# Kernel optimization log

Measured on AMD Instinct MI355X. Metric: run time of the kernel, lower is better.

Reference implementation:

```python
import jax, jax.numpy as jnp
import numpy as np

N = 100000
E = 1600000
IN_DIM, FEAT, HID, OUT = 128, 64, 64, 64


def setup_inputs() -> dict:
    key = jax.random.key(0)
    ks = jax.random.split(key, 12)
    x = jax.random.normal(ks[0], (N, IN_DIM), dtype=jnp.float32)
    edge_index = jax.random.randint(ks[1], (2, E), 0, N, dtype=jnp.int64)
    def lin(k, fan_in, fan_out):
        s = 1.0 / np.sqrt(fan_in)
        kw, kb = jax.random.split(k)
        W = jax.random.uniform(kw, (fan_in, fan_out), jnp.float32, -s, s)
        b = jax.random.uniform(kb, (fan_out,), jnp.float32, -s, s)
        return W, b
    W_pre, b_pre = lin(ks[2], IN_DIM, FEAT)
    W1, b1 = lin(ks[3], FEAT, HID)
    Wh, bh = lin(ks[4], HID, HID)
    Wo, bo = lin(ks[5], HID, OUT)
    return {"x": x, "edge_index": edge_index,
            "W_pre": W_pre, "b_pre": b_pre,
            "W1": W1, "b1": b1, "Wh": Wh, "bh": bh,
            "Wo": Wo, "bo": bo}


def _gcn_conv(x, W, b, src, dst, norm, n):
    # linear transform then normalized scatter-add aggregation at dst
    h = x @ W                           # [N, out]
    msg = h[src] * norm[:, None]        # [E+N, out] gather + scale
    out = jax.ops.segment_sum(msg, dst, num_segments=n)
    return out + b


def reference(x, edge_index, W_pre, b_pre, W1, b1, Wh, bh, Wo, bo):
    n = x.shape[0]
    loop = jnp.arange(n, dtype=edge_index.dtype)
    src = jnp.concatenate([edge_index[0], loop])  # self-loops appended
    dst = jnp.concatenate([edge_index[1], loop])
    deg = jax.ops.segment_sum(jnp.ones_like(dst, x.dtype), dst, num_segments=n)
    dinv = jnp.where(deg > 0, jax.lax.rsqrt(deg), 0.0)
    norm = dinv[src] * dinv[dst]        # symmetric D^-1/2 A_hat D^-1/2

    h = x @ W_pre + b_pre               # feature_pre linear
    h = jax.nn.relu(_gcn_conv(h, W1, b1, src, dst, norm, n))
    # dropout is identity in eval mode
    h = jax.nn.relu(_gcn_conv(h, Wh, bh, src, dst, norm, n))
    h = _gcn_conv(h, Wo, bo, src, dst, norm, n)
    # row-wise L2 normalize (F.normalize, eps=1e-12)
    nrm = jnp.maximum(jnp.linalg.norm(h, axis=-1, keepdims=True), 1e-12)
    return h / nrm
```

## Files before the change

kernel.cpp:

```cpp
#include <hip/hip_runtime.h>
#include <hip/hip_fp16.h>

#define N_DIM 128
#define F_DIM 64
#define NB 256
#define TILE 2048
#define BCAP 8192

typedef _Float16 half8 __attribute__((ext_vector_type(8)));
typedef float f32x4 __attribute__((ext_vector_type(4)));

__global__ __launch_bounds__(256) void k_compose(const float* __restrict__ Wpre, const float* __restrict__ W1,
                                                 const float* __restrict__ bpre, float* __restrict__ Wc,
                                                 float* __restrict__ bb) {
    int c = threadIdx.x & 63;
    int rq = threadIdx.x >> 6;
    for (int r = rq; r < N_DIM; r += 4) {
        float acc = 0.f;
        for (int k = 0; k < 64; ++k) acc = fmaf(Wpre[r * 64 + k], W1[k * 64 + c], acc);
        Wc[r * 64 + c] = acc;
    }
    if (rq == 0) {
        float acc = 0.f;
        for (int k = 0; k < 64; ++k) acc = fmaf(bpre[k], W1[k * 64 + c], acc);
        bb[c] = acc;
    }
}

__global__ __launch_bounds__(256) void k_bucket(const int* __restrict__ src, const int* __restrict__ dst,
                                                int* __restrict__ bsrc, int* __restrict__ bdst,
                                                int* __restrict__ bcnt, int e, unsigned int magic, int cap) {
    __shared__ int hist[NB], lofs[NB], gbase[NB], lcur[NB];
    __shared__ int as_[TILE], ad_[TILE];
    __shared__ unsigned char ab_[TILE];
    int tid = threadIdx.x;
    for (int t0 = blockIdx.x * TILE; t0 < e; t0 += gridDim.x * TILE) {
        int cnt = min(TILE, e - t0);
        hist[tid] = 0;
        __syncthreads();
        int dv[8], sv[8], bv[8];
#pragma unroll
        for (int j = 0; j < 8; ++j) {
            int local = j * 256 + tid;
            int idx = t0 + local;
            bool ok = local < cnt;
            dv[j] = ok ? __builtin_nontemporal_load(dst + idx) : 0;
            sv[j] = ok ? __builtin_nontemporal_load(src + idx) : 0;
            bv[j] = ok ? (int)(((unsigned long long)(unsigned)dv[j] * magic) >> 32) : -1;
            if (ok) atomicAdd(&hist[bv[j]], 1);
        }
        __syncthreads();
        int v = hist[tid];
        lofs[tid] = v;
        __syncthreads();
        for (int o = 1; o < NB; o <<= 1) {
            int x = (tid >= o) ? lofs[tid - o] : 0;
            __syncthreads();
            lofs[tid] += x;
            __syncthreads();
        }
        int excl = lofs[tid] - v;
        lofs[tid] = excl;
        lcur[tid] = excl;
        gbase[tid] = atomicAdd(&bcnt[tid], v);
        __syncthreads();
#pragma unroll
        for (int j = 0; j < 8; ++j) {
            if (bv[j] >= 0) {
                int pos = atomicAdd(&lcur[bv[j]], 1);
                as_[pos] = sv[j];
                ad_[pos] = dv[j];
                ab_[pos] = (unsigned char)bv[j];
            }
        }
        __syncthreads();
        for (int k = tid; k < cnt; k += 256) {
            int p = ab_[k];
            size_t gi = (size_t)p * cap + gbase[p] + (k - lofs[p]);
            bsrc[gi] = as_[k];
            bdst[gi] = ad_[k];
        }
        __syncthreads();
    }
}

__global__ __launch_bounds__(256) void k_sort(const int* __restrict__ bsrc, const int* __restrict__ bdst,
                                              const int* __restrict__ bcnt,
                                              float* __restrict__ dinv, int* __restrict__ start,
                                              int* __restrict__ srcs, int cap, int nchunk, int n, int e) {
    __shared__ int sb[NB];
    __shared__ int lcnt[512], lcur[512];
    __shared__ int out[BCAP];
    int t = threadIdx.x;
    int b = blockIdx.x;
    int bc = bcnt[t];
    sb[t] = bc;
    __syncthreads();
    for (int o = 1; o < NB; o <<= 1) {
        int x = (t >= o) ? sb[t - o] : 0;
        __syncthreads();
        sb[t] += x;
        __syncthreads();
    }
    int base = sb[b] - bcnt[b];
    if (b == 0 && t == 0) start[n] = e;
    __syncthreads();

    int len = min(bcnt[b], min(cap, BCAP));
    int d0 = b * nchunk;
    int nloc = min(nchunk, n - d0);
    lcnt[t] = 0; lcnt[t + 256] = 0;
    __syncthreads();
    const int* bd = bdst + (size_t)b * cap;
    const int* bs = bsrc + (size_t)b * cap;
    for (int i = t; i < len; i += 256) atomicAdd(&lcnt[bd[i] - d0], 1);
    __syncthreads();
    int sv0 = lcnt[t], sv1 = lcnt[t + 256];
    for (int o = 1; o < 512; o <<= 1) {
        int x0 = (t >= o) ? lcnt[t - o] : 0;
        int x1 = (t + 256 >= o) ? lcnt[t + 256 - o] : 0;
        __syncthreads();
        lcnt[t] += x0;
        lcnt[t + 256] += x1;
        __syncthreads();
    }
    int ex0 = lcnt[t] - sv0;
    int ex1 = lcnt[t + 256] - sv1;
    lcur[t] = ex0; lcur[t + 256] = ex1;
    if (t < nloc) { start[d0 + t] = base + ex0; dinv[d0 + t] = rsqrtf((float)sv0 + 1.0f); }
    if (t + 256 < nloc) { start[d0 + t + 256] = base + ex1; dinv[d0 + t + 256] = rsqrtf((float)sv1 + 1.0f); }
    __syncthreads();
    for (int i = t; i < len; i += 256) {
        int d = bd[i] - d0;
        int pos = atomicAdd(&lcur[d], 1);
        out[pos] = bs[i];
    }
    __syncthreads();
    for (int k = t; k < len; k += 256) srcs[base + k] = out[k];
}


template <int S>
__device__ inline void pack_w(const float* __restrict__ W, half8* __restrict__ Bf) {
    for (int f = threadIdx.x; f < S * 4 * 64; f += 256) {
        int l = f & 63, c = (f >> 6) & 3, s = f >> 8;
        int kbase = s * 32 + ((l >> 4) << 3);
        int col = c * 16 + (l & 15);
        half8 pk;
#pragma unroll
        for (int i = 0; i < 8; ++i) pk[i] = (_Float16)W[(kbase + i) * 64 + col];
        Bf[f] = pk;
    }
    __syncthreads();
}

__global__ __launch_bounds__(256) void k_gemm_f(const float* __restrict__ X, const float* __restrict__ Wc,
                                                const float* __restrict__ bb, const float* __restrict__ dinv,
                                                __half* __restrict__ U, int n) {
    __shared__ half8 Bf[4 * 4 * 64];
    pack_w<4>(Wc, Bf);
    int lane = threadIdx.x & 63;
    int row = lane & 15, kq = lane >> 4;
    float bbv0 = bb[0 * 16 + row], bbv1 = bb[1 * 16 + row], bbv2 = bb[2 * 16 + row], bbv3 = bb[3 * 16 + row];
    int gw = (blockIdx.x * 256 + threadIdx.x) >> 6;
    int nw = (gridDim.x * 256) >> 6;
    int ntile = n >> 4;
    for (int tile = gw; tile < ntile; tile += nw) {
        int r0 = tile << 4;
        const float* xp = X + (size_t)(r0 + row) * N_DIM + (kq << 3);
        f32x4 ac0 = {0.f, 0.f, 0.f, 0.f}, ac1 = ac0, ac2 = ac0, ac3 = ac0;
#pragma unroll
        for (int s = 0; s < 4; ++s) {
            float4 lo = *(const float4*)(xp + s * 32);
            float4 hi = *(const float4*)(xp + s * 32 + 4);
            half8 a;
            a[0] = (_Float16)lo.x; a[1] = (_Float16)lo.y; a[2] = (_Float16)lo.z; a[3] = (_Float16)lo.w;
            a[4] = (_Float16)hi.x; a[5] = (_Float16)hi.y; a[6] = (_Float16)hi.z; a[7] = (_Float16)hi.w;
            ac0 = __builtin_amdgcn_mfma_f32_16x16x32_f16(a, Bf[(s * 4 + 0) * 64 + lane], ac0, 0, 0, 0);
            ac1 = __builtin_amdgcn_mfma_f32_16x16x32_f16(a, Bf[(s * 4 + 1) * 64 + lane], ac1, 0, 0, 0);
            ac2 = __builtin_amdgcn_mfma_f32_16x16x32_f16(a, Bf[(s * 4 + 2) * 64 + lane], ac2, 0, 0, 0);
            ac3 = __builtin_amdgcn_mfma_f32_16x16x32_f16(a, Bf[(s * 4 + 3) * 64 + lane], ac3, 0, 0, 0);
        }
        int rbase = r0 + (kq << 2);
        float d0 = dinv[rbase + 0], d1 = dinv[rbase + 1], d2 = dinv[rbase + 2], d3 = dinv[rbase + 3];
        __half* up = U + (size_t)rbase * F_DIM + row;
        up[0 * F_DIM +  0] = __float2half(d0 * (ac0[0] + bbv0));
        up[1 * F_DIM +  0] = __float2half(d1 * (ac0[1] + bbv0));
        up[2 * F_DIM +  0] = __float2half(d2 * (ac0[2] + bbv0));
        up[3 * F_DIM +  0] = __float2half(d3 * (ac0[3] + bbv0));
        up[0 * F_DIM + 16] = __float2half(d0 * (ac1[0] + bbv1));
        up[1 * F_DIM + 16] = __float2half(d1 * (ac1[1] + bbv1));
        up[2 * F_DIM + 16] = __float2half(d2 * (ac1[2] + bbv1));
        up[3 * F_DIM + 16] = __float2half(d3 * (ac1[3] + bbv1));
        up[0 * F_DIM + 32] = __float2half(d0 * (ac2[0] + bbv2));
        up[1 * F_DIM + 32] = __float2half(d1 * (ac2[1] + bbv2));
        up[2 * F_DIM + 32] = __float2half(d2 * (ac2[2] + bbv2));
        up[3 * F_DIM + 32] = __float2half(d3 * (ac2[3] + bbv2));
        up[0 * F_DIM + 48] = __float2half(d0 * (ac3[0] + bbv3));
        up[1 * F_DIM + 48] = __float2half(d1 * (ac3[1] + bbv3));
        up[2 * F_DIM + 48] = __float2half(d2 * (ac3[2] + bbv3));
        up[3 * F_DIM + 48] = __float2half(d3 * (ac3[3] + bbv3));
    }
}

__global__ __launch_bounds__(256) void k_gemm_l(const __half* __restrict__ H, const float* __restrict__ W,
                                                const float* __restrict__ dinv, __half* __restrict__ U, int n) {
    __shared__ half8 Bf[2 * 4 * 64];
    pack_w<2>(W, Bf);
    int lane = threadIdx.x & 63;
    int row = lane & 15, kq = lane >> 4;
    int gw = (blockIdx.x * 256 + threadIdx.x) >> 6;
    int nw = (gridDim.x * 256) >> 6;
    int ntile = n >> 4;
    for (int tile = gw; tile < ntile; tile += nw) {
        int r0 = tile << 4;
        const _Float16* hp = (const _Float16*)H + (size_t)(r0 + row) * F_DIM + (kq << 3);
        half8 a0 = *(const half8*)(hp);
        half8 a1 = *(const half8*)(hp + 32);
        f32x4 ac0 = {0.f, 0.f, 0.f, 0.f}, ac1 = ac0, ac2 = ac0, ac3 = ac0;
        ac0 = __builtin_amdgcn_mfma_f32_16x16x32_f16(a0, Bf[0 * 64 + lane], ac0, 0, 0, 0);
        ac1 = __builtin_amdgcn_mfma_f32_16x16x32_f16(a0, Bf[1 * 64 + lane], ac1, 0, 0, 0);
        ac2 = __builtin_amdgcn_mfma_f32_16x16x32_f16(a0, Bf[2 * 64 + lane], ac2, 0, 0, 0);
        ac3 = __builtin_amdgcn_mfma_f32_16x16x32_f16(a0, Bf[3 * 64 + lane], ac3, 0, 0, 0);
        ac0 = __builtin_amdgcn_mfma_f32_16x16x32_f16(a1, Bf[4 * 64 + lane], ac0, 0, 0, 0);
        ac1 = __builtin_amdgcn_mfma_f32_16x16x32_f16(a1, Bf[5 * 64 + lane], ac1, 0, 0, 0);
        ac2 = __builtin_amdgcn_mfma_f32_16x16x32_f16(a1, Bf[6 * 64 + lane], ac2, 0, 0, 0);
        ac3 = __builtin_amdgcn_mfma_f32_16x16x32_f16(a1, Bf[7 * 64 + lane], ac3, 0, 0, 0);
        int rbase = r0 + (kq << 2);
        float d0 = dinv[rbase + 0], d1 = dinv[rbase + 1], d2 = dinv[rbase + 2], d3 = dinv[rbase + 3];
        __half* up = U + (size_t)rbase * F_DIM + row;
        up[0 * F_DIM +  0] = __float2half(d0 * ac0[0]);
        up[1 * F_DIM +  0] = __float2half(d1 * ac0[1]);
        up[2 * F_DIM +  0] = __float2half(d2 * ac0[2]);
        up[3 * F_DIM +  0] = __float2half(d3 * ac0[3]);
        up[0 * F_DIM + 16] = __float2half(d0 * ac1[0]);
        up[1 * F_DIM + 16] = __float2half(d1 * ac1[1]);
        up[2 * F_DIM + 16] = __float2half(d2 * ac1[2]);
        up[3 * F_DIM + 16] = __float2half(d3 * ac1[3]);
        up[0 * F_DIM + 32] = __float2half(d0 * ac2[0]);
        up[1 * F_DIM + 32] = __float2half(d1 * ac2[1]);
        up[2 * F_DIM + 32] = __float2half(d2 * ac2[2]);
        up[3 * F_DIM + 32] = __float2half(d3 * ac2[3]);
        up[0 * F_DIM + 48] = __float2half(d0 * ac3[0]);
        up[1 * F_DIM + 48] = __float2half(d1 * ac3[1]);
        up[2 * F_DIM + 48] = __float2half(d2 * ac3[2]);
        up[3 * F_DIM + 48] = __float2half(d3 * ac3[3]);
    }
}


#define PKADD(ACC, V)                                             \
    {                                                             \
        const __half2* _hp = (const __half2*)&(V);                \
        ACC[0] = __hadd2(ACC[0], _hp[0]);                         \
        ACC[1] = __hadd2(ACC[1], _hp[1]);                         \
        ACC[2] = __hadd2(ACC[2], _hp[2]);                         \
        ACC[3] = __hadd2(ACC[3], _hp[3]);                         \
    }

template <int MODE>
__global__ __launch_bounds__(256) void k_agg(const __half* __restrict__ U, const int* __restrict__ srcs,
                                             const int* __restrict__ start, const float* __restrict__ dinv,
                                             const float* __restrict__ bias, void* __restrict__ outp, int n) {
    int lane = threadIdx.x & 63;
    int g = lane >> 3;
    int t = lane & 7;
    int node = ((blockIdx.x << 2) + (threadIdx.x >> 6)) * 8 + g;
    if (node >= n) return;
    const float4* U4 = (const float4*)U;

    int s0 = start[node];
    int s1 = start[node + 1];

    float4 sv = U4[(size_t)node * 8 + t];
    __half2 acc[4];
    acc[0] = ((const __half2*)&sv)[0];
    acc[1] = ((const __half2*)&sv)[1];
    acc[2] = ((const __half2*)&sv)[2];
    acc[3] = ((const __half2*)&sv)[3];

    float4 z = make_float4(0.f, 0.f, 0.f, 0.f);
    int idxA[8];
#pragma unroll
    for (int j = 0; j < 8; ++j) idxA[j] = (s0 + j < s1) ? srcs[s0 + j] : 0;
    for (int p = s0; p < s1; p += 8) {
        float4 vv[8];
#pragma unroll
        for (int j = 0; j < 8; ++j)
            vv[j] = (p + j < s1) ? U4[(size_t)idxA[j] * 8 + t] : z;
        int pn = p + 8;
#pragma unroll
        for (int j = 0; j < 8; ++j)
            idxA[j] = (pn + j < s1) ? srcs[pn + j] : 0;
#pragma unroll
        for (int j = 0; j < 8; ++j) PKADD(acc, vv[j]);
    }

    float2 f0 = __half22float2(acc[0]);
    float2 f1 = __half22float2(acc[1]);
    float2 f2 = __half22float2(acc[2]);
    float2 f3 = __half22float2(acc[3]);

    float di = dinv[node];
    const float4* b4 = (const float4*)bias;
    float4 bv0 = b4[2 * t], bv1 = b4[2 * t + 1];
    float v[8];
    v[0] = fmaf(di, f0.x, bv0.x); v[1] = fmaf(di, f0.y, bv0.y);
    v[2] = fmaf(di, f1.x, bv0.z); v[3] = fmaf(di, f1.y, bv0.w);
    v[4] = fmaf(di, f2.x, bv1.x); v[5] = fmaf(di, f2.y, bv1.y);
    v[6] = fmaf(di, f3.x, bv1.z); v[7] = fmaf(di, f3.y, bv1.w);

    if (MODE == 0) {
        __half hr[8];
#pragma unroll
        for (int j = 0; j < 8; ++j) hr[j] = __float2half(fmaxf(v[j], 0.f));
        *(float4*)((__half*)outp + (size_t)node * F_DIM + t * 8) = *(float4*)hr;
    } else {
        float ss = 0.f;
#pragma unroll
        for (int j = 0; j < 8; ++j) ss = fmaf(v[j], v[j], ss);
        ss += __shfl_xor(ss, 1);
        ss += __shfl_xor(ss, 2);
        ss += __shfl_xor(ss, 4);
        float inv = 1.0f / fmaxf(sqrtf(ss), 1e-12f);
        float4 r0, r1;
        r0.x = v[0] * inv; r0.y = v[1] * inv; r0.z = v[2] * inv; r0.w = v[3] * inv;
        r1.x = v[4] * inv; r1.y = v[5] * inv; r1.z = v[6] * inv; r1.w = v[7] * inv;
        float4* o4 = (float4*)((float*)outp + (size_t)node * F_DIM);
        o4[2 * t] = r0; o4[2 * t + 1] = r1;
    }
}


extern "C" void kernel_launch(void* const* d_in, const int* in_sizes, int n_in,
                              void* d_out, int out_size, void* d_ws, size_t ws_size,
                              hipStream_t stream) {
    const float* x     = (const float*)d_in[0];
    const int*   ei    = (const int*)d_in[1];
    const float* W_pre = (const float*)d_in[2];
    const float* b_pre = (const float*)d_in[3];
    const float* W1    = (const float*)d_in[4];
    const float* b1    = (const float*)d_in[5];
    const float* Wh    = (const float*)d_in[6];
    const float* bh    = (const float*)d_in[7];
    const float* Wo    = (const float*)d_in[8];
    const float* bo    = (const float*)d_in[9];

    int n = in_sizes[0] / N_DIM;
    int e = in_sizes[1] / 2;
    const int* srcIdx = ei;
    const int* dstIdx = ei + e;

    size_t off = 0;
    auto alloc = [&](size_t bytes) -> void* {
        void* p = (char*)d_ws + off;
        off += (bytes + 255) & ~(size_t)255;
        return p;
    };
    int cap = BCAP;

    int*    start  = (int*)alloc((size_t)(n + 1) * 4);
    float*  dinv   = (float*)alloc((size_t)n * 4);
    int*    bcnt   = (int*)alloc(NB * 4);
    int*    srcs   = (int*)alloc((size_t)e * 4);
    int*    bsrc   = (int*)alloc((size_t)NB * cap * 4);
    int*    bdst   = (int*)alloc((size_t)NB * cap * 4);
    __half* h      = (__half*)alloc((size_t)n * F_DIM * 2);
    __half* u      = (__half*)alloc((size_t)n * F_DIM * 2);
    float*  Wc     = (float*)alloc((size_t)N_DIM * 64 * 4);
    float*  bb     = (float*)alloc(64 * 4);

    int nbAgg = (n + 31) / 32;
    int nchunk = (n + NB - 1) / NB;
    unsigned int magic = (unsigned int)(((1ull << 32) + nchunk - 1) / nchunk);

    k_compose<<<1, 256, 0, stream>>>(W_pre, W1, b_pre, Wc, bb);

    hipMemsetAsync(bcnt, 0, NB * 4, stream);
    int nbTile = (e + TILE - 1) / TILE;
    k_bucket<<<nbTile, 256, 0, stream>>>(srcIdx, dstIdx, bsrc, bdst, bcnt, e, magic, cap);

    k_sort<<<NB, 256, 0, stream>>>(bsrc, bdst, bcnt, dinv, start, srcs, cap, nchunk, n, e);

    k_gemm_f<<<800, 256, 0, stream>>>(x, Wc, bb, dinv, u, n);
    k_agg<0><<<nbAgg, 256, 0, stream>>>(u, srcs, start, dinv, b1, h, n);

    k_gemm_l<<<800, 256, 0, stream>>>(h, Wh, dinv, u, n);
    k_agg<0><<<nbAgg, 256, 0, stream>>>(u, srcs, start, dinv, bh, h, n);

    k_gemm_l<<<800, 256, 0, stream>>>(h, Wo, dinv, u, n);
    k_agg<1><<<nbAgg, 256, 0, stream>>>(u, srcs, start, dinv, bo, d_out, n);
}
```

Before: 284.9 us.

## Fuse next-layer GEMM into aggregation epilogue and fold bcnt memset into compose

New measurement: 422.3 us. 48.2% more time.

```diff
diff --git a/kernel.cpp b/kernel.cpp
--- a/kernel.cpp
+++ b/kernel.cpp
@@ -12,7 +12,8 @@
 
 __global__ __launch_bounds__(256) void k_compose(const float* __restrict__ Wpre, const float* __restrict__ W1,
                                                  const float* __restrict__ bpre, float* __restrict__ Wc,
-                                                 float* __restrict__ bb) {
+                                                 float* __restrict__ bb, int* __restrict__ bcnt) {
+    bcnt[threadIdx.x] = 0;
     int c = threadIdx.x & 63;
     int rq = threadIdx.x >> 6;
     for (int r = rq; r < N_DIM; r += 4) {
@@ -203,51 +204,6 @@
     }
 }
 
-__global__ __launch_bounds__(256) void k_gemm_l(const __half* __restrict__ H, const float* __restrict__ W,
-                                                const float* __restrict__ dinv, __half* __restrict__ U, int n) {
-    __shared__ half8 Bf[2 * 4 * 64];
-    pack_w<2>(W, Bf);
-    int lane = threadIdx.x & 63;
-    int row = lane & 15, kq = lane >> 4;
-    int gw = (blockIdx.x * 256 + threadIdx.x) >> 6;
-    int nw = (gridDim.x * 256) >> 6;
-    int ntile = n >> 4;
-    for (int tile = gw; tile < ntile; tile += nw) {
-        int r0 = tile << 4;
-        const _Float16* hp = (const _Float16*)H + (size_t)(r0 + row) * F_DIM + (kq << 3);
-        half8 a0 = *(const half8*)(hp);
-        half8 a1 = *(const half8*)(hp + 32);
-        f32x4 ac0 = {0.f, 0.f, 0.f, 0.f}, ac1 = ac0, ac2 = ac0, ac3 = ac0;
-        ac0 = __builtin_amdgcn_mfma_f32_16x16x32_f16(a0, Bf[0 * 64 + lane], ac0, 0, 0, 0);
-        ac1 = __builtin_amdgcn_mfma_f32_16x16x32_f16(a0, Bf[1 * 64 + lane], ac1, 0, 0, 0);
-        ac2 = __builtin_amdgcn_mfma_f32_16x16x32_f16(a0, Bf[2 * 64 + lane], ac2, 0, 0, 0);
-        ac3 = __builtin_amdgcn_mfma_f32_16x16x32_f16(a0, Bf[3 * 64 + lane], ac3, 0, 0, 0);
-        ac0 = __builtin_amdgcn_mfma_f32_16x16x32_f16(a1, Bf[4 * 64 + lane], ac0, 0, 0, 0);
-        ac1 = __builtin_amdgcn_mfma_f32_16x16x32_f16(a1, Bf[5 * 64 + lane], ac1, 0, 0, 0);
-        ac2 = __builtin_amdgcn_mfma_f32_16x16x32_f16(a1, Bf[6 * 64 + lane], ac2, 0, 0, 0);
-        ac3 = __builtin_amdgcn_mfma_f32_16x16x32_f16(a1, Bf[7 * 64 + lane], ac3, 0, 0, 0);
-        int rbase = r0 + (kq << 2);
-        float d0 = dinv[rbase + 0], d1 = dinv[rbase + 1], d2 = dinv[rbase + 2], d3 = dinv[rbase + 3];
-        __half* up = U + (size_t)rbase * F_DIM + row;
-        up[0 * F_DIM +  0] = __float2half(d0 * ac0[0]);
-        up[1 * F_DIM +  0] = __float2half(d1 * ac0[1]);
-        up[2 * F_DIM +  0] = __float2half(d2 * ac0[2]);
-        up[3 * F_DIM +  0] = __float2half(d3 * ac0[3]);
-        up[0 * F_DIM + 16] = __float2half(d0 * ac1[0]);
-        up[1 * F_DIM + 16] = __float2half(d1 * ac1[1]);
-        up[2 * F_DIM + 16] = __float2half(d2 * ac1[2]);
-        up[3 * F_DIM + 16] = __float2half(d3 * ac1[3]);
-        up[0 * F_DIM + 32] = __float2half(d0 * ac2[0]);
-        up[1 * F_DIM + 32] = __float2half(d1 * ac2[1]);
-        up[2 * F_DIM + 32] = __float2half(d2 * ac2[2]);
-        up[3 * F_DIM + 32] = __float2half(d3 * ac2[3]);
-        up[0 * F_DIM + 48] = __float2half(d0 * ac3[0]);
-        up[1 * F_DIM + 48] = __float2half(d1 * ac3[1]);
-        up[2 * F_DIM + 48] = __float2half(d2 * ac3[2]);
-        up[3 * F_DIM + 48] = __float2half(d3 * ac3[3]);
-    }
-}
-
 
 #define PKADD(ACC, V)                                             \
     {                                                             \
@@ -261,7 +217,13 @@
 template <int MODE>
 __global__ __launch_bounds__(256) void k_agg(const __half* __restrict__ U, const int* __restrict__ srcs,
                                              const int* __restrict__ start, const float* __restrict__ dinv,
-                                             const float* __restrict__ bias, void* __restrict__ outp, int n) {
+                                             const float* __restrict__ bias, const float* __restrict__ Wn,
+                                             void* __restrict__ outp, int n) {
+    __shared__ __half Wl[64 * 64];
+    if (MODE == 0) {
+        for (int i = threadIdx.x; i < 64 * 64; i += 256) Wl[i] = __float2half(Wn[i]);
+        __syncthreads();
+    }
     int lane = threadIdx.x & 63;
     int g = lane >> 3;
     int t = lane & 7;
@@ -311,9 +273,30 @@
     v[6] = fmaf(di, f3.x, bv1.z); v[7] = fmaf(di, f3.y, bv1.w);
 
     if (MODE == 0) {
+        float hv[8];
+#pragma unroll
+        for (int j = 0; j < 8; ++j) hv[j] = fmaxf(v[j], 0.f);
+        float ua[8] = {0.f, 0.f, 0.f, 0.f, 0.f, 0.f, 0.f, 0.f};
+#pragma unroll
+        for (int j = 0; j < 8; ++j) {
+            float myv = hv[j];
+#pragma unroll
+            for (int ls = 0; ls < 8; ++ls) {
+                float hk = __shfl(myv, (g << 3) | ls);
+                int k = ls * 8 + j;
+                float4 wq = *(const float4*)(Wl + k * 64 + t * 8);
+                const __half2* wp = (const __half2*)&wq;
+                float2 w0 = __half22float2(wp[0]), w1 = __half22float2(wp[1]);
+                float2 w2 = __half22float2(wp[2]), w3 = __half22float2(wp[3]);
+                ua[0] = fmaf(hk, w0.x, ua[0]); ua[1] = fmaf(hk, w0.y, ua[1]);
+                ua[2] = fmaf(hk, w1.x, ua[2]); ua[3] = fmaf(hk, w1.y, ua[3]);
+                ua[4] = fmaf(hk, w2.x, ua[4]); ua[5] = fmaf(hk, w2.y, ua[5]);
+                ua[6] = fmaf(hk, w3.x, ua[6]); ua[7] = fmaf(hk, w3.y, ua[7]);
+            }
+        }
         __half hr[8];
 #pragma unroll
-        for (int j = 0; j < 8; ++j) hr[j] = __float2half(fmaxf(v[j], 0.f));
+        for (int j = 0; j < 8; ++j) hr[j] = __float2half(di * ua[j]);
         *(float4*)((__half*)outp + (size_t)node * F_DIM + t * 8) = *(float4*)hr;
     } else {
         float ss = 0.f;
@@ -365,8 +348,8 @@
     int*    srcs   = (int*)alloc((size_t)e * 4);
     int*    bsrc   = (int*)alloc((size_t)NB * cap * 4);
     int*    bdst   = (int*)alloc((size_t)NB * cap * 4);
-    __half* h      = (__half*)alloc((size_t)n * F_DIM * 2);
-    __half* u      = (__half*)alloc((size_t)n * F_DIM * 2);
+    __half* uA     = (__half*)alloc((size_t)n * F_DIM * 2);
+    __half* uB     = (__half*)alloc((size_t)n * F_DIM * 2);
     float*  Wc     = (float*)alloc((size_t)N_DIM * 64 * 4);
     float*  bb     = (float*)alloc(64 * 4);
 
@@ -374,20 +357,18 @@
     int nchunk = (n + NB - 1) / NB;
     unsigned int magic = (unsigned int)(((1ull << 32) + nchunk - 1) / nchunk);
 
-    k_compose<<<1, 256, 0, stream>>>(W_pre, W1, b_pre, Wc, bb);
-
-    hipMemsetAsync(bcnt, 0, NB * 4, stream);
+    k_compose<<<1, 256, 0, stream>>>(W_pre, W1, b_pre, Wc, bb, bcnt);
+
     int nbTile = (e + TILE - 1) / TILE;
     k_bucket<<<nbTile, 256, 0, stream>>>(srcIdx, dstIdx, bsrc, bdst, bcnt, e, magic, cap);
 
     k_sort<<<NB, 256, 0, stream>>>(bsrc, bdst, bcnt, dinv, start, srcs, cap, nchunk, n, e);
 
-    k_gemm_f<<<800, 256, 0, stream>>>(x, Wc, bb, dinv, u, n);
-    k_agg<0><<<nbAgg, 256, 0, stream>>>(u, srcs, start, dinv, b1, h, n);
-
-    k_gemm_l<<<800, 256, 0, stream>>>(h, Wh, dinv, u, n);
-    k_agg<0><<<nbAgg, 256, 0, stream>>>(u, srcs, start, dinv, bh, h, n);
-
-    k_gemm_l<<<800, 256, 0, stream>>>(h, Wo, dinv, u, n);
-    k_agg<1><<<nbAgg, 256, 0, stream>>>(u, srcs, start, dinv, bo, d_out, n);
-}
+    k_gemm_f<<<800, 256, 0, stream>>>(x, Wc, bb, dinv, uA, n);
+
+    k_agg<0><<<nbAgg, 256, 0, stream>>>(uA, srcs, start, dinv, b1, Wh, uB, n);
+
+    k_agg<0><<<nbAgg, 256, 0, stream>>>(uB, srcs, start, dinv, bh, Wo, uA, n);
+
+    k_agg<1><<<nbAgg, 256, 0, stream>>>(uA, srcs, start, dinv, bo, nullptr, d_out, n);
+}
```
